# Kernel tuning notes

Hardware: AMD Instinct MI355X
Metric: run time of the kernel (lower is better)

## Reference

```python
import jax, jax.numpy as jnp
import numpy as np

H, C = 5, 64            # attention heads, per-head channels (out_channels=conv_dim)
NEG_SLOPE = 0.2         # GATv2 leaky_relu slope
N_NODES = 50000

def setup_inputs() -> dict:
    key = jax.random.key(0)
    ks = jax.random.split(key, 10)
    N, E = N_NODES, 400000
    node_dim, edge_dim = 128, 16
    s = 0.1
    return {
        'x': jax.random.normal(ks[0], (N, node_dim), jnp.float32),
        'edge_index': jax.random.randint(ks[1], (2, E), 0, N),
        'edge_attr': jax.random.normal(ks[2], (E, edge_dim), jnp.float32),
        'W0': jax.random.normal(ks[3], (node_dim, H * C), jnp.float32) * s,
        'b0': jnp.zeros((H * C,), jnp.float32),
        'We0': jax.random.normal(ks[4], (edge_dim, H * C), jnp.float32) * s,
        'att0': jax.random.normal(ks[5], (H, C), jnp.float32) * s,
        'bias0': jnp.zeros((C,), jnp.float32),
        'W12': jax.random.normal(ks[6], (2, C, H * C), jnp.float32) * s,
        'b12': jnp.zeros((2, H * C), jnp.float32),
        'We12': jax.random.normal(ks[7], (2, edge_dim, H * C), jnp.float32) * s,
        'att12': jax.random.normal(ks[8], (2, H, C), jnp.float32) * s,
        'bias12': jnp.zeros((2, C), jnp.float32),
    }

def _add_self_loops_mean(edge_index, edge_attr, N):
    # PyG add_self_loops(fill_value='mean'): self-loop attr = mean of incoming edge attrs per dst node
    dst = edge_index[1]
    sums = jax.ops.segment_sum(edge_attr, dst, num_segments=N)
    cnt = jax.ops.segment_sum(jnp.ones((edge_attr.shape[0], 1), edge_attr.dtype), dst, num_segments=N)
    loop_attr = sums / jnp.maximum(cnt, 1.0)
    loop = jnp.arange(N, dtype=edge_index.dtype)
    ei = jnp.concatenate([edge_index, jnp.stack([loop, loop])], axis=1)
    ea = jnp.concatenate([edge_attr, loop_attr], axis=0)
    return ei, ea

def _gatv2_layer(x, src, dst, eattr, W, b, We, att, bias, N):
    h = (x @ W + b).reshape(N, H, C)                     # shared lin_l==lin_r (share_weights=True)
    e = (eattr @ We).reshape(-1, H, C)                   # lin_edge (no bias)
    s = jax.nn.leaky_relu(h[src] + h[dst] + e, NEG_SLOPE)  # [E', H, C]
    logits = jnp.einsum('ehc,hc->eh', s, att)            # [E', H]
    m = jax.ops.segment_max(logits, dst, num_segments=N)
    m = jnp.where(jnp.isfinite(m), m, 0.0)
    ex = jnp.exp(logits - m[dst])
    denom = jax.ops.segment_sum(ex, dst, num_segments=N) + 1e-16
    alpha = ex / denom[dst]                              # per-dst softmax (dropout off: eval mode)
    msg = h[src] * alpha[:, :, None]
    out = jax.ops.segment_sum(msg, dst, num_segments=N)  # [N, H, C]
    return out.mean(axis=1) + bias                       # concat=False -> head mean, then bias

def reference(x, edge_index, edge_attr, W0, b0, We0, att0, bias0, W12, b12, We12, att12, bias12):
    N = x.shape[0]
    ei, ea = _add_self_loops_mean(edge_index, edge_attr, N)
    src, dst = ei[0], ei[1]
    h = jax.nn.elu(_gatv2_layer(x, src, dst, ea, W0, b0, We0, att0, bias0, N))
    for i in range(2):
        h = jax.nn.elu(_gatv2_layer(h, src, dst, ea, W12[i], b12[i], We12[i], att12[i], bias12[i], N))
    return h  # jk_mode='last'
```

## Files before the change

kernel.cpp:

```cpp
#include <hip/hip_runtime.h>
#include <hip/hip_fp16.h>
#include <math.h>

#define NH 5
#define NC 64
#define ED 16
#define HC 320
#define CH 32

typedef _Float16 h2  __attribute__((ext_vector_type(2)));
typedef _Float16 v8h __attribute__((ext_vector_type(8)));
typedef float    v4f __attribute__((ext_vector_type(4)));

template<int ctrl, int rmask>
__device__ __forceinline__ float dpp_add(float x) {
    int y = __builtin_amdgcn_update_dpp(0, __float_as_int(x), ctrl, rmask, 0xf, true);
    return x + __int_as_float(y);
}
__device__ __forceinline__ float wave_sum_all(float x) {
    x = dpp_add<0xb1, 0xf>(x);
    x = dpp_add<0x4e, 0xf>(x);
    x = dpp_add<0x114, 0xf>(x);
    x = dpp_add<0x118, 0xf>(x);
    x = dpp_add<0x142, 0xa>(x);
    x = dpp_add<0x143, 0xc>(x);
    return __int_as_float(__builtin_amdgcn_readlane(__float_as_int(x), 63));
}


__global__ void count_kernel(const int* __restrict__ dst, int* __restrict__ cnt, int E) {
    int t = blockIdx.x * blockDim.x + threadIdx.x;
    if (t >= E) return;
    atomicAdd(&cnt[dst[t]], 1);
}

__global__ void scan_kernel(const int* __restrict__ cnt, int* __restrict__ offsets,
                            int* __restrict__ cursor, int N) {
    __shared__ int sums[1024];
    int t = threadIdx.x;
    int chunk = (N + 1023) / 1024;
    int beg = t * chunk;
    int end = min(beg + chunk, N);
    int s = 0;
    for (int i = beg; i < end; ++i) s += cnt[i] + 1;
    sums[t] = s;
    __syncthreads();
    for (int o = 1; o < 1024; o <<= 1) {
        int v = (t >= o) ? sums[t - o] : 0;
        __syncthreads();
        sums[t] += v;
        __syncthreads();
    }
    int run = (t > 0) ? sums[t - 1] : 0;
    for (int i = beg; i < end; ++i) {
        offsets[i] = run; cursor[i] = run;
        run += cnt[i] + 1;
    }
    if (t == 0) offsets[N] = sums[1023];
}

__global__ void scatter_kernel(const int* __restrict__ src, const int* __restrict__ dst,
                               int* __restrict__ cursor, int2* __restrict__ recs, int N, int E) {
    int t = blockIdx.x * blockDim.x + threadIdx.x;
    if (t >= E + N) return;
    int d, s;
    if (t < E) { d = dst[t]; s = src[t]; }
    else       { d = t - E; s = t - E; }
    int pos = atomicAdd(&cursor[d], 1);
    recs[pos] = make_int2(s, t);
}

__global__ void loop_from_csr(const int* __restrict__ offsets, const int2* __restrict__ recs,
                              const float* __restrict__ ea, float* __restrict__ loop,
                              int N, int E) {
    int t = blockIdx.x * blockDim.x + threadIdx.x;
    int n = t >> 4, k = t & 15;
    if (n >= N) return;
    int beg = offsets[n], end = offsets[n + 1];
    float s = 0.f; int c = 0;
    for (int j = beg; j < end; ++j) {
        int y = recs[j].y;
        if (y < E) { s += ea[(size_t)y * ED + k]; ++c; }
    }
    loop[(size_t)n * ED + k] = s / (float)max(c, 1);
}

__global__ void reorder_ea(const int2* __restrict__ recs, const float* __restrict__ ea,
                           const float* __restrict__ loop, h2* __restrict__ easrt,
                           int R, int E) {
    int t = blockIdx.x * blockDim.x + threadIdx.x;
    int slot = t >> 3, k2 = t & 7;
    if (slot >= R) return;
    int y = recs[slot].y;
    const float2* sp = (const float2*)((y < E) ? ea + (size_t)y * ED : loop + (size_t)(y - E) * ED);
    float2 f = sp[k2];
    h2 o; o.x = (_Float16)f.x; o.y = (_Float16)f.y;
    easrt[(size_t)slot * 8 + k2] = o;
}

__global__ void win_start_kernel(const int* __restrict__ offsets, int* __restrict__ winStart, int N) {
    int i = blockIdx.x * blockDim.x + threadIdx.x;
    if (i >= N) return;
    atomicMin(&winStart[offsets[i] / CH], i);
}

__global__ void cvt_f16(const float* __restrict__ in, _Float16* __restrict__ out, int n) {
    int i = blockIdx.x * blockDim.x + threadIdx.x;
    if (i < n) out[i] = (_Float16)in[i];
}

__global__ void transpose_w(const float* __restrict__ W, _Float16* __restrict__ Wt, int K) {
    int t = blockIdx.x * blockDim.x + threadIdx.x;
    if (t >= 320 * K) return;
    int k = t / 320, n = t % 320;
    Wt[(size_t)n * K + k] = (_Float16)W[t];
}

__global__ __launch_bounds__(256) void gemm_mfma(const _Float16* __restrict__ A,
                                                 const _Float16* __restrict__ Bt,
                                                 const float* __restrict__ bias,
                                                 _Float16* __restrict__ Cout, int M, int K) {
    int lane = threadIdx.x & 63;
    int wave = threadIdx.x >> 6;
    int m = lane & 15, quad = lane >> 4;
    int rowBase = (blockIdx.x * 4 + wave) * 16;
    if (rowBase >= M) return;

    v4f acc[20];
#pragma unroll
    for (int c = 0; c < 20; ++c) acc[c] = (v4f){0.f, 0.f, 0.f, 0.f};

    for (int k0 = 0; k0 < K; k0 += 32) {
        v8h a = *(const v8h*)&A[(size_t)(rowBase + m) * K + k0 + quad * 8];
#pragma unroll
        for (int c = 0; c < 20; ++c) {
            v8h b = *(const v8h*)&Bt[(size_t)(c * 16 + m) * K + k0 + quad * 8];
            acc[c] = __builtin_amdgcn_mfma_f32_16x16x32_f16(a, b, acc[c], 0, 0, 0);
        }
    }
#pragma unroll
    for (int c = 0; c < 20; ++c) {
        float bb = bias[c * 16 + m];
#pragma unroll
        for (int r = 0; r < 4; ++r) {
            int row = rowBase + quad * 4 + r;
            Cout[(size_t)row * HC + c * 16 + m] = (_Float16)(acc[c][r] + bb);
        }
    }
}

__global__ __launch_bounds__(256) void gat_fused(const _Float16* __restrict__ hbuf,
                                                 const int* __restrict__ offsets,
                                                 const int2* __restrict__ recs,
                                                 const h2* __restrict__ easrt,
                                                 const int* __restrict__ winStart,
                                                 const float* __restrict__ We,
                                                 const float* __restrict__ att,
                                                 const float* __restrict__ bias,
                                                 _Float16* __restrict__ outH,
                                                 float* __restrict__ outF,
                                                 int N, int R) {
    int lane = threadIdx.x & 63;
    int wave = (blockIdx.x * blockDim.x + threadIdx.x) >> 6;
    int totalWaves = (gridDim.x * blockDim.x) >> 6;

    h2 we2[8 * NH];
#pragma unroll
    for (int k2 = 0; k2 < 8; ++k2)
#pragma unroll
        for (int h = 0; h < NH; ++h) {
            h2 w;
            w.x = (_Float16)We[(2 * k2) * HC + h * NC + lane];
            w.y = (_Float16)We[(2 * k2 + 1) * HC + h * NC + lane];
            we2[k2 * NH + h] = w;
        }
    float attc6[NH], attc4[NH];
#pragma unroll
    for (int h = 0; h < NH; ++h) {
        float a = att[h * NC + lane];
        attc6[h] = 0.6f * a;
        attc4[h] = 0.4f * a;
    }
    float bc = bias[lane];

    for (int w = wave; w * CH < R; w += totalWaves) {
        int i = winStart[w];
        if (i >= N) continue;
        int winEnd = w * CH + CH;
        for (; i < N; ++i) {
            int beg = offsets[i];
            if (beg >= winEnd) break;
            int end = offsets[i + 1];

            const _Float16* dp = hbuf + (size_t)i * HC + lane;
            float hd[NH];
#pragma unroll
            for (int h = 0; h < NH; ++h) hd[h] = (float)dp[h * NC];

            float l[NH] = {}, acc[NH] = {};
            for (int t = beg; t < end; ++t) {
                int src = recs[t].x;
                const h2* ap = easrt + (size_t)t * 8;
                h2 a[8];
#pragma unroll
                for (int k2 = 0; k2 < 8; ++k2) a[k2] = ap[k2];
                const _Float16* sp = hbuf + (size_t)src * HC + lane;
                float hs[NH];
#pragma unroll
                for (int h = 0; h < NH; ++h) hs[h] = (float)sp[h * NC];

                float p[NH];
#pragma unroll
                for (int h = 0; h < NH; ++h) {
                    float v = hs[h] + hd[h];
#pragma unroll
                    for (int k2 = 0; k2 < 8; ++k2)
                        v = __builtin_amdgcn_fdot2(a[k2], we2[k2 * NH + h], v, false);
                    p[h] = fmaf(fabsf(v), attc4[h], v * attc6[h]);
                }
#pragma unroll
                for (int h = 0; h < NH; ++h) {
                    float pe = __expf(wave_sum_all(p[h]));
                    l[h] += pe;
                    acc[h] = fmaf(pe, hs[h], acc[h]);
                }
            }
            float o = 0.f;
#pragma unroll
            for (int h = 0; h < NH; ++h) o += acc[h] / l[h];
            o = o * 0.2f + bc;
            o = o > 0.f ? o : expm1f(o);
            if (outF) outF[(size_t)i * NC + lane] = o;
            else      outH[(size_t)i * NC + lane] = (_Float16)o;
        }
    }
}

extern "C" void kernel_launch(void* const* d_in, const int* in_sizes, int n_in,
                              void* d_out, int out_size, void* d_ws, size_t ws_size,
                              hipStream_t stream) {
    const float* x     = (const float*)d_in[0];
    const int*   ei    = (const int*)d_in[1];
    const float* ea    = (const float*)d_in[2];
    const float* W0    = (const float*)d_in[3];
    const float* b0    = (const float*)d_in[4];
    const float* We0   = (const float*)d_in[5];
    const float* att0  = (const float*)d_in[6];
    const float* bias0 = (const float*)d_in[7];
    const float* W12   = (const float*)d_in[8];
    const float* b12   = (const float*)d_in[9];
    const float* We12  = (const float*)d_in[10];
    const float* att12 = (const float*)d_in[11];
    const float* bias12= (const float*)d_in[12];

    int N = in_sizes[0] / 128;
    int E = in_sizes[1] / 2;
    int R = E + N;
    int numWin = (R + CH - 1) / CH;
    const int* srcArr = ei;
    const int* dstArr = ei + E;

    char* ws = (char*)d_ws;
    size_t off = 0;
    auto alloc = [&](size_t bytes) -> void* {
        void* p = ws + off;
        off = (off + bytes + 255) & ~(size_t)255;
        return p;
    };
    int*      cnt     = (int*)alloc((size_t)N * 4);
    int*      offsets = (int*)alloc((size_t)(N + 1) * 4);
    int*      cursor  = (int*)alloc((size_t)N * 4);
    int2*     recs    = (int2*)alloc((size_t)R * 8);
    float*    loop    = (float*)alloc((size_t)N * ED * 4);
    _Float16* hbuf    = (_Float16*)alloc((size_t)N * HC * 2);
    _Float16* acth    = (_Float16*)alloc((size_t)N * NC * 2);
    _Float16* xh      = (_Float16*)alloc((size_t)N * 128 * 2);
    _Float16* Wth0    = (_Float16*)alloc((size_t)320 * 128 * 2);
    _Float16* Wth1    = (_Float16*)alloc((size_t)320 * 64 * 2);
    _Float16* Wth2    = (_Float16*)alloc((size_t)320 * 64 * 2);
    int*      winStart= (int*)alloc((size_t)(numWin + 1) * 4);
    h2*       easrt   = (h2*)alloc((size_t)R * 32);

    (void)hipMemsetAsync(cnt, 0, (size_t)N * 4, stream);
    (void)hipMemsetAsync(winStart, 0x7f, (size_t)(numWin + 1) * 4, stream);
    count_kernel<<<(E + 255) / 256, 256, 0, stream>>>(dstArr, cnt, E);
    scan_kernel<<<1, 1024, 0, stream>>>(cnt, offsets, cursor, N);
    scatter_kernel<<<(E + N + 255) / 256, 256, 0, stream>>>(srcArr, dstArr, cursor, recs, N, E);
    loop_from_csr<<<((size_t)N * ED + 255) / 256, 256, 0, stream>>>(offsets, recs, ea, loop, N, E);
    reorder_ea<<<((size_t)R * 8 + 255) / 256, 256, 0, stream>>>(recs, ea, loop, easrt, R, E);
    win_start_kernel<<<(N + 255) / 256, 256, 0, stream>>>(offsets, winStart, N);
    cvt_f16<<<((size_t)N * 128 + 255) / 256, 256, 0, stream>>>(x, xh, N * 128);
    transpose_w<<<(320 * 128 + 255) / 256, 256, 0, stream>>>(W0, Wth0, 128);
    transpose_w<<<(320 * 64 + 255) / 256, 256, 0, stream>>>(W12, Wth1, 64);
    transpose_w<<<(320 * 64 + 255) / 256, 256, 0, stream>>>(W12 + 64 * HC, Wth2, 64);

    float* dout = (float*)d_out;
    int gemmBlocks = (N / 16 + 3) / 4 + 1;
    int fusedBlocks = 2048;

    const _Float16* As[3]  = {xh, acth, acth};
    const _Float16* Bts[3] = {Wth0, Wth1, Wth2};
    int Ks[3] = {128, 64, 64};
    const float* bs[3]   = {b0, b12, b12 + HC};
    const float* Wes[3]  = {We0, We12, We12 + ED * HC};
    const float* atts[3] = {att0, att12, att12 + NH * NC};
    const float* bis[3]  = {bias0, bias12, bias12 + NC};
    for (int layer = 0; layer < 3; ++layer) {
        gemm_mfma<<<gemmBlocks, 256, 0, stream>>>(As[layer], Bts[layer], bs[layer], hbuf, N, Ks[layer]);
        gat_fused<<<fusedBlocks, 256, 0, stream>>>(hbuf, offsets, recs, easrt, winStart,
                                                   Wes[layer], atts[layer], bis[layer],
                                                   acth, (layer == 2) ? dout : nullptr, N, R);
    }
}
```

Measured before the change: 870.5 us.

## Interleave heads in hbuf, unroll edge loop by two, compact src indices

Changes the projected-feature buffer layout so each node stores its five head values per channel contiguously, padded to eight halves. The GEMM epilogue writes one vector per channel and the attention kernel reads each neighbour row with a single 16-byte load instead of five strided ones. The edge loop is unrolled by two so more independent gathers and reductions can be in flight, and it reads a packed int source array instead of the 8-byte record array. exp is switched to exp2 with log2(e) folded into the attention weights, and the grid is sized to cover the number of windows. The cost is about 60% more hbuf footprint and traffic from the padding, plus a little extra preprocessing to build the source array.

```diff
diff --git a/kernel.cpp b/kernel.cpp
--- a/kernel.cpp
+++ b/kernel.cpp
@@ -87,11 +87,13 @@
 
 __global__ void reorder_ea(const int2* __restrict__ recs, const float* __restrict__ ea,
                            const float* __restrict__ loop, h2* __restrict__ easrt,
-                           int R, int E) {
+                           int* __restrict__ srcs, int R, int E) {
     int t = blockIdx.x * blockDim.x + threadIdx.x;
     int slot = t >> 3, k2 = t & 7;
     if (slot >= R) return;
-    int y = recs[slot].y;
+    int2 rc = recs[slot];
+    if (k2 == 0) srcs[slot] = rc.x;
+    int y = rc.y;
     const float2* sp = (const float2*)((y < E) ? ea + (size_t)y * ED : loop + (size_t)(y - E) * ED);
     float2 f = sp[k2];
     h2 o; o.x = (_Float16)f.x; o.y = (_Float16)f.y;
@@ -138,20 +140,28 @@
             acc[c] = __builtin_amdgcn_mfma_f32_16x16x32_f16(a, b, acc[c], 0, 0, 0);
         }
     }
-#pragma unroll
-    for (int c = 0; c < 20; ++c) {
-        float bb = bias[c * 16 + m];
-#pragma unroll
-        for (int r = 0; r < 4; ++r) {
-            int row = rowBase + quad * 4 + r;
-            Cout[(size_t)row * HC + c * 16 + m] = (_Float16)(acc[c][r] + bb);
+    float bb[20];
+#pragma unroll
+    for (int c = 0; c < 20; ++c) bb[c] = bias[c * 16 + m];
+#pragma unroll
+    for (int r = 0; r < 4; ++r) {
+        int row = rowBase + quad * 4 + r;
+#pragma unroll
+        for (int c03 = 0; c03 < 4; ++c03) {
+            v8h o = {};
+#pragma unroll
+            for (int h = 0; h < NH; ++h) {
+                int c = c03 + 4 * h;
+                o[h] = (_Float16)(acc[c][r] + bb[c]);
+            }
+            *(v8h*)&Cout[(((size_t)row) * 64 + c03 * 16 + m) * 8] = o;
         }
     }
 }
 
 __global__ __launch_bounds__(256) void gat_fused(const _Float16* __restrict__ hbuf,
                                                  const int* __restrict__ offsets,
-                                                 const int2* __restrict__ recs,
+                                                 const int* __restrict__ srcs,
                                                  const h2* __restrict__ easrt,
                                                  const int* __restrict__ winStart,
                                                  const float* __restrict__ We,
@@ -163,6 +173,7 @@
     int lane = threadIdx.x & 63;
     int wave = (blockIdx.x * blockDim.x + threadIdx.x) >> 6;
     int totalWaves = (gridDim.x * blockDim.x) >> 6;
+    const float L2E = 1.4426950408889634f;
 
     h2 we2[8 * NH];
 #pragma unroll
@@ -178,8 +189,8 @@
 #pragma unroll
     for (int h = 0; h < NH; ++h) {
         float a = att[h * NC + lane];
-        attc6[h] = 0.6f * a;
-        attc4[h] = 0.4f * a;
+        attc6[h] = 0.6f * L2E * a;
+        attc4[h] = 0.4f * L2E * a;
     }
     float bc = bias[lane];
 
@@ -192,37 +203,63 @@
             if (beg >= winEnd) break;
             int end = offsets[i + 1];
 
-            const _Float16* dp = hbuf + (size_t)i * HC + lane;
+            v8h hdv = *(const v8h*)&hbuf[((size_t)i * 64 + lane) * 8];
             float hd[NH];
 #pragma unroll
-            for (int h = 0; h < NH; ++h) hd[h] = (float)dp[h * NC];
+            for (int h = 0; h < NH; ++h) hd[h] = (float)hdv[h];
 
             float l[NH] = {}, acc[NH] = {};
-            for (int t = beg; t < end; ++t) {
-                int src = recs[t].x;
+            int t = beg;
+            for (; t + 2 <= end; t += 2) {
+                int s0 = srcs[t], s1 = srcs[t + 1];
+                v8h hs0v = *(const v8h*)&hbuf[((size_t)s0 * 64 + lane) * 8];
+                v8h hs1v = *(const v8h*)&hbuf[((size_t)s1 * 64 + lane) * 8];
                 const h2* ap = easrt + (size_t)t * 8;
-                h2 a[8];
-#pragma unroll
-                for (int k2 = 0; k2 < 8; ++k2) a[k2] = ap[k2];
-                const _Float16* sp = hbuf + (size_t)src * HC + lane;
-                float hs[NH];
-#pragma unroll
-                for (int h = 0; h < NH; ++h) hs[h] = (float)sp[h * NC];
-
-                float p[NH];
+                h2 a0[8], a1[8];
+#pragma unroll
+                for (int k2 = 0; k2 < 8; ++k2) { a0[k2] = ap[k2]; a1[k2] = ap[8 + k2]; }
+                float hs0[NH], hs1[NH], p0[NH], p1[NH];
+#pragma unroll
+                for (int h = 0; h < NH; ++h) { hs0[h] = (float)hs0v[h]; hs1[h] = (float)hs1v[h]; }
 #pragma unroll
                 for (int h = 0; h < NH; ++h) {
-                    float v = hs[h] + hd[h];
+                    float v0 = hs0[h] + hd[h];
+                    float v1 = hs1[h] + hd[h];
+#pragma unroll
+                    for (int k2 = 0; k2 < 8; ++k2) {
+                        v0 = __builtin_amdgcn_fdot2(a0[k2], we2[k2 * NH + h], v0, false);
+                        v1 = __builtin_amdgcn_fdot2(a1[k2], we2[k2 * NH + h], v1, false);
+                    }
+                    p0[h] = fmaf(fabsf(v0), attc4[h], v0 * attc6[h]);
+                    p1[h] = fmaf(fabsf(v1), attc4[h], v1 * attc6[h]);
+                }
+#pragma unroll
+                for (int h = 0; h < NH; ++h) {
+                    float pe0 = exp2f(wave_sum_all(p0[h]));
+                    float pe1 = exp2f(wave_sum_all(p1[h]));
+                    l[h] += pe0 + pe1;
+                    acc[h] = fmaf(pe0, hs0[h], fmaf(pe1, hs1[h], acc[h]));
+                }
+            }
+            if (t < end) {
+                int s0 = srcs[t];
+                v8h hs0v = *(const v8h*)&hbuf[((size_t)s0 * 64 + lane) * 8];
+                const h2* ap = easrt + (size_t)t * 8;
+                h2 a0[8];
+#pragma unroll
+                for (int k2 = 0; k2 < 8; ++k2) a0[k2] = ap[k2];
+                float hs0[NH];
+#pragma unroll
+                for (int h = 0; h < NH; ++h) hs0[h] = (float)hs0v[h];
+#pragma unroll
+                for (int h = 0; h < NH; ++h) {
+                    float v0 = hs0[h] + hd[h];
 #pragma unroll
                     for (int k2 = 0; k2 < 8; ++k2)
-                        v = __builtin_amdgcn_fdot2(a[k2], we2[k2 * NH + h], v, false);
-                    p[h] = fmaf(fabsf(v), attc4[h], v * attc6[h]);
-                }
-#pragma unroll
-                for (int h = 0; h < NH; ++h) {
-                    float pe = __expf(wave_sum_all(p[h]));
-                    l[h] += pe;
-                    acc[h] = fmaf(pe, hs[h], acc[h]);
+                        v0 = __builtin_amdgcn_fdot2(a0[k2], we2[k2 * NH + h], v0, false);
+                    float pe0 = exp2f(wave_sum_all(fmaf(fabsf(v0), attc4[h], v0 * attc6[h])));
+                    l[h] += pe0;
+                    acc[h] = fmaf(pe0, hs0[h], acc[h]);
                 }
             }
             float o = 0.f;
@@ -272,7 +309,7 @@
     int*      cursor  = (int*)alloc((size_t)N * 4);
     int2*     recs    = (int2*)alloc((size_t)R * 8);
     float*    loop    = (float*)alloc((size_t)N * ED * 4);
-    _Float16* hbuf    = (_Float16*)alloc((size_t)N * HC * 2);
+    _Float16* hbuf    = (_Float16*)alloc((size_t)N * 64 * 8 * 2);
     _Float16* acth    = (_Float16*)alloc((size_t)N * NC * 2);
     _Float16* xh      = (_Float16*)alloc((size_t)N * 128 * 2);
     _Float16* Wth0    = (_Float16*)alloc((size_t)320 * 128 * 2);
@@ -280,6 +317,7 @@
     _Float16* Wth2    = (_Float16*)alloc((size_t)320 * 64 * 2);
     int*      winStart= (int*)alloc((size_t)(numWin + 1) * 4);
     h2*       easrt   = (h2*)alloc((size_t)R * 32);
+    int*      srcs    = (int*)alloc((size_t)R * 4);
 
     (void)hipMemsetAsync(cnt, 0, (size_t)N * 4, stream);
     (void)hipMemsetAsync(winStart, 0x7f, (size_t)(numWin + 1) * 4, stream);
@@ -287,7 +325,7 @@
     scan_kernel<<<1, 1024, 0, stream>>>(cnt, offsets, cursor, N);
     scatter_kernel<<<(E + N + 255) / 256, 256, 0, stream>>>(srcArr, dstArr, cursor, recs, N, E);
     loop_from_csr<<<((size_t)N * ED + 255) / 256, 256, 0, stream>>>(offsets, recs, ea, loop, N, E);
-    reorder_ea<<<((size_t)R * 8 + 255) / 256, 256, 0, stream>>>(recs, ea, loop, easrt, R, E);
+    reorder_ea<<<((size_t)R * 8 + 255) / 256, 256, 0, stream>>>(recs, ea, loop, easrt, srcs, R, E);
     win_start_kernel<<<(N + 255) / 256, 256, 0, stream>>>(offsets, winStart, N);
     cvt_f16<<<((size_t)N * 128 + 255) / 256, 256, 0, stream>>>(x, xh, N * 128);
     transpose_w<<<(320 * 128 + 255) / 256, 256, 0, stream>>>(W0, Wth0, 128);
@@ -296,7 +334,7 @@
 
     float* dout = (float*)d_out;
     int gemmBlocks = (N / 16 + 3) / 4 + 1;
-    int fusedBlocks = 2048;
+    int fusedBlocks = (numWin + 3) / 4;
 
     const _Float16* As[3]  = {xh, acth, acth};
     const _Float16* Bts[3] = {Wth0, Wth1, Wth2};
@@ -307,7 +345,7 @@
     const float* bis[3]  = {bias0, bias12, bias12 + NC};
     for (int layer = 0; layer < 3; ++layer) {
         gemm_mfma<<<gemmBlocks, 256, 0, stream>>>(As[layer], Bts[layer], bs[layer], hbuf, N, Ks[layer]);
-        gat_fused<<<fusedBlocks, 256, 0, stream>>>(hbuf, offsets, recs, easrt, winStart,
+        gat_fused<<<fusedBlocks, 256, 0, stream>>>(hbuf, offsets, srcs, easrt, winStart,
                                                    Wes[layer], atts[layer], bis[layer],
                                                    acth, (layer == 2) ? dout : nullptr, N, R);
     }
```

Result: slower. 890.5 us (+2.3%).
